# Optimization experiments

Hardware: AMD Instinct MI355X
Metric: run time of the kernel (lower is better)

The kernel has to match this reference:

```python
import jax, jax.numpy as jnp
import numpy as np

B, N, C, K = 4, 1024, 384, 10


def _sqdist(a, b):
    # a: [B,P,3], b: [B,M,3] -> [B,P,M] squared euclidean distance
    d = (jnp.sum(a * a, -1)[:, :, None] + jnp.sum(b * b, -1)[:, None, :]
         - 2.0 * jnp.einsum('bpc,bmc->bpm', a, b))
    return jnp.maximum(d, 0.0)


def _gather(points, idx):
    # points: [B,M,C], idx: [B,...] int -> [B,...,C]  (index_points)
    return jax.vmap(lambda p, i: p[i])(points, idx)


def setup_inputs() -> dict:
    key = jax.random.key(0)
    ks = jax.random.split(key, 8)
    def lin(k_, fan_in, fan_out):
        return jax.random.normal(k_, (fan_in, fan_out), jnp.float32) * (1.0 / np.sqrt(fan_in))
    return {
        'q': jax.random.normal(ks[0], (B, N, C), jnp.float32),
        'q_pos': jax.random.normal(ks[1], (B, N, 3), jnp.float32),
        'Wv': lin(ks[2], C, C), 'bv': jnp.zeros((C,), jnp.float32),
        'W1': lin(ks[3], 2 * C, C), 'b1': jnp.zeros((C,), jnp.float32),
        'ln_g': jnp.ones((C,), jnp.float32), 'ln_b': jnp.zeros((C,), jnp.float32),
        'W2': lin(ks[4], C, 3),
        'Wk': lin(ks[5], 2 * C, C), 'bk': jnp.zeros((C,), jnp.float32),
    }


def reference(q, q_pos, Wv, bv, W1, b1, ln_g, ln_b, W2, Wk, bk):
    Bq, Nq, Cq = q.shape
    # 1) KNN of each query among all points (self-attn: v=q, v_pos=q_pos)
    d = _sqdist(q_pos, q_pos)                      # [B,N,N]
    _, idx = jax.lax.top_k(-d, K)                  # [B,N,K] (smallest distances)
    # 2) offset prediction from gathered projected features + query feature
    v_off = q @ Wv + bv                            # [B,N,C]
    off_local_v = _gather(v_off, idx)              # [B,N,K,C]
    qk = jnp.broadcast_to(q[:, :, None, :], (Bq, Nq, K, Cq))
    shift_feat = jnp.concatenate([off_local_v, qk], -1)  # [B,N,K,2C]
    h = shift_feat @ W1 + b1
    mu = jnp.mean(h, -1, keepdims=True)
    var = jnp.var(h, -1, keepdims=True)
    h = (h - mu) / jnp.sqrt(var + 1e-5) * ln_g + ln_b     # LayerNorm
    h = jax.nn.gelu(h, approximate=False)
    offset = jnp.tanh(h @ W2)                      # [B,N,K,3]
    # 3) deformed positions, scaled by half the local bbox extent
    local_v_pos = _gather(q_pos, idx)              # [B,N,K,3]
    scale = (local_v_pos.max(-2) - local_v_pos.min(-2))[:, :, None, :] * 0.5
    shift_pos = (local_v_pos + offset * scale).reshape(Bq, Nq * K, 3)
    # 4) three_nn + three_interpolate (inverse-squared-distance weights)
    d2 = _sqdist(shift_pos, q_pos)                 # [B,NK,N]
    negd, idx3 = jax.lax.top_k(-d2, 3)             # [B,NK,3]
    dist = -negd
    w = 1.0 / (dist + 1e-8)
    w = w / jnp.sum(w, -1, keepdims=True)
    feats3 = _gather(q, idx3)                      # [B,NK,3,C]
    interp = jnp.einsum('bpt,bptc->bpc', w, feats3).reshape(Bq, Nq, K, Cq)
    # 5) graph conv: concat(diff, q) -> Linear -> LeakyReLU(0.2) -> max over K
    feature = jnp.concatenate([interp - qk, qk], -1)      # [B,N,K,2C]
    out = jax.nn.leaky_relu(feature @ Wk + bk, negative_slope=0.2)
    return out.max(-2)                             # [B,N,C]
```

## Files before the change

### kernel.cpp

```cpp
#include <hip/hip_runtime.h>
#include <math.h>

#define BB 4
#define NN 1024
#define CC 384
#define KK 10
#define NKK (NN*KK)

typedef __attribute__((ext_vector_type(8))) short short8v;
typedef __attribute__((ext_vector_type(8))) unsigned short ushort8v;
typedef __attribute__((ext_vector_type(4))) float f32x4;

template <int NA>
__device__ __forceinline__ void wave_sum_arr(float* a) {
  #pragma unroll
  for (int off = 32; off > 0; off >>= 1) {
    float t[NA];
    #pragma unroll
    for (int u = 0; u < NA; ++u) t[u] = __shfl_xor(a[u], off, 64);
    #pragma unroll
    for (int u = 0; u < NA; ++u) a[u] += t[u];
  }
}

__device__ __forceinline__ unsigned short f2bf(float x) {
  unsigned int b = __float_as_uint(x);
  return (unsigned short)((b + 0x7fffu + ((b >> 16) & 1u)) >> 16);
}
__device__ __forceinline__ float bf2f(unsigned short h) {
  return __uint_as_float(((unsigned int)h) << 16);
}

#define NB_CVT  (BB * NN * CC / 1024)
#define NB_PB   (2 * CC * CC / 256)
#define NB_PREP (NB_CVT + NB_PB + 3)
__global__ __launch_bounds__(256) void prep_gemm_kernel(
    const float* __restrict__ q,
    const float* __restrict__ W1, const float* __restrict__ b1,
    const float* __restrict__ bv, const float* __restrict__ bk,
    const float* __restrict__ Wk, const float* __restrict__ Wv,
    unsigned short* __restrict__ qh, unsigned short* __restrict__ ql,
    unsigned short* __restrict__ Wt,
    float* __restrict__ bias_uv, float* __restrict__ bias_pb,
    float* __restrict__ M1p) {
  int blk = blockIdx.x;
  int tid = threadIdx.x;
  if (blk < NB_CVT) {
    int i = (blk * 256 + tid) * 4;
    float4 v = *reinterpret_cast<const float4*>(q + i);
    float x[4] = {v.x, v.y, v.z, v.w};
    #pragma unroll
    for (int j = 0; j < 4; ++j) {
      unsigned short h = f2bf(x[j]);
      qh[i + j] = h;
      ql[i + j] = f2bf(x[j] - bf2f(h));
    }
    return;
  }
  if (blk < NB_CVT + NB_PB) {
    int idx = (blk - NB_CVT) * 256 + tid;
    int n = idx / CC, k = idx % CC;
    float v;
    if (n < CC) v = Wk[(size_t)k * CC + n];
    else        v = Wk[(size_t)CC * CC + k * CC + (n - CC)] - Wk[(size_t)k * CC + (n - CC)];
    Wt[(size_t)n * CC + k] = f2bf(v);
    return;
  }
  if (blk < NB_PREP) {
    int j = (blk - NB_CVT - NB_PB) * 256 + tid;
    if (j >= 2 * CC) return;
    if (j < CC) { bias_uv[j] = 0.f; bias_pb[j] = 0.f; }
    else {
      int c = j - CC;
      float s = b1[c];
      for (int i = 0; i < CC; ++i) s += bv[i] * W1[i * CC + c];
      bias_uv[j] = s;
      bias_pb[j] = bk[c];
    }
    return;
  }
  {
    int r = blk - NB_PREP;
    int bx = r % 3, by = (r / 3) % 3, bz = r / 9;
    __shared__ float As[16][132];
    __shared__ float Bs[16][128];
    int tx = tid & 15, ty = tid >> 4;
    int row0 = by * 128, col0 = bx * 128;
    int k0 = bz * 48;
    float acc[8][8] = {};
    int arow = tid >> 2, akc = (tid & 3) << 2;
    int brow = tid >> 5, bcol = (tid & 31) << 2;
    for (int kt = k0; kt < k0 + 48; kt += 16) {
      #pragma unroll
      for (int h = 0; h < 2; ++h) {
        int rr = arow + 64 * h;
        float4 av = *reinterpret_cast<const float4*>(Wv + (size_t)(row0 + rr) * CC + kt + akc);
        As[akc + 0][rr] = av.x; As[akc + 1][rr] = av.y;
        As[akc + 2][rr] = av.z; As[akc + 3][rr] = av.w;
      }
      #pragma unroll
      for (int h = 0; h < 2; ++h) {
        int rr = brow + 8 * h;
        float4 bv4 = *reinterpret_cast<const float4*>(W1 + (size_t)(kt + rr) * CC + col0 + bcol);
        *reinterpret_cast<float4*>(&Bs[rr][bcol]) = bv4;
      }
      __syncthreads();
      #pragma unroll
      for (int kk = 0; kk < 16; ++kk) {
        float4 a0 = *reinterpret_cast<const float4*>(&As[kk][ty << 2]);
        float4 a1 = *reinterpret_cast<const float4*>(&As[kk][64 + (ty << 2)]);
        float4 b0 = *reinterpret_cast<const float4*>(&Bs[kk][tx << 2]);
        float4 b1 = *reinterpret_cast<const float4*>(&Bs[kk][64 + (tx << 2)]);
        float av_[8] = {a0.x, a0.y, a0.z, a0.w, a1.x, a1.y, a1.z, a1.w};
        float bv_[8] = {b0.x, b0.y, b0.z, b0.w, b1.x, b1.y, b1.z, b1.w};
        #pragma unroll
        for (int i = 0; i < 8; ++i)
          #pragma unroll
          for (int j = 0; j < 8; ++j) acc[i][j] += av_[i] * bv_[j];
      }
      __syncthreads();
    }
    float* Cz = M1p + (size_t)bz * CC * CC;
    #pragma unroll
    for (int i = 0; i < 8; ++i) {
      int row = row0 + (ty << 2) + (i & 3) + ((i & 4) << 4);
      if (row >= CC) continue;
      #pragma unroll
      for (int h = 0; h < 2; ++h) {
        int col = col0 + 64 * h + (tx << 2);
        if (col >= CC) continue;
        float4 rv;
        rv.x = acc[i][4 * h + 0]; rv.y = acc[i][4 * h + 1];
        rv.z = acc[i][4 * h + 2]; rv.w = acc[i][4 * h + 3];
        *reinterpret_cast<float4*>(Cz + (size_t)row * CC + col) = rv;
      }
    }
  }
}

__global__ void pack_uv_split_kernel(const float* __restrict__ M1p, const float* __restrict__ W1,
                                     unsigned short* __restrict__ Buvh,
                                     unsigned short* __restrict__ Buvl) {
  int idx = blockIdx.x * 256 + threadIdx.x;
  int k = idx / (2 * CC), n = idx % (2 * CC);
  float val;
  if (n < CC) {
    float s = 0.f;
    #pragma unroll
    for (int p = 0; p < 8; ++p) s += M1p[(size_t)p * CC * CC + (size_t)k * CC + n];
    val = s;
  } else {
    val = W1[(size_t)(CC + k) * CC + (n - CC)];
  }
  unsigned short h = f2bf(val);
  Buvh[(size_t)n * CC + k] = h;
  Buvl[(size_t)n * CC + k] = f2bf(val - bf2f(h));
}

__global__ __launch_bounds__(256) void gemm_mfma_kernel(
    const unsigned short* __restrict__ qh, const unsigned short* __restrict__ ql,
    const unsigned short* __restrict__ Buvh, const unsigned short* __restrict__ Buvl,
    const unsigned short* __restrict__ Wt,
    float* __restrict__ Cuv, float* __restrict__ Cpb,
    const float* __restrict__ bias_uv, const float* __restrict__ bias_pb) {
  int path = blockIdx.z;
  const unsigned short* Bh = path ? Wt : Buvh;
  float* Cm = path ? Cpb : Cuv;
  const float* bias = path ? bias_pb : bias_uv;
  __shared__ unsigned short Ah[128 * 32], Alo[128 * 32];
  __shared__ unsigned short Bhs[128 * 32], Bls[128 * 32];
  int tid = threadIdx.x;
  int lane = tid & 63, w = tid >> 6;
  int m0 = blockIdx.y * 128, n0 = blockIdx.x * 128;
  f32x4 acc[4][4];
  #pragma unroll
  for (int i = 0; i < 4; ++i)
    #pragma unroll
    for (int j = 0; j < 4; ++j) acc[i][j] = (f32x4){0.f, 0.f, 0.f, 0.f};
  int rl = lane & 15, kg = lane >> 4;
  for (int k0 = 0; k0 < CC; k0 += 32) {
    #pragma unroll
    for (int j = 0; j < 2; ++j) {
      int id = tid + 256 * j;
      int r = id >> 2, s = id & 3;
      int sw = (s ^ (r & 3)) * 8;
      *reinterpret_cast<ushort8v*>(Ah + r * 32 + sw) =
          *reinterpret_cast<const ushort8v*>(qh + (size_t)(m0 + r) * CC + k0 + s * 8);
      *reinterpret_cast<ushort8v*>(Bhs + r * 32 + sw) =
          *reinterpret_cast<const ushort8v*>(Bh + (size_t)(n0 + r) * CC + k0 + s * 8);
      if (!path) {
        *reinterpret_cast<ushort8v*>(Alo + r * 32 + sw) =
            *reinterpret_cast<const ushort8v*>(ql + (size_t)(m0 + r) * CC + k0 + s * 8);
        *reinterpret_cast<ushort8v*>(Bls + r * 32 + sw) =
            *reinterpret_cast<const ushort8v*>(Buvl + (size_t)(n0 + r) * CC + k0 + s * 8);
      }
    }
    __syncthreads();
    short8v afh[4], bfh[4], afl[4], bfl[4];
    #pragma unroll
    for (int f = 0; f < 4; ++f) {
      int ar = (w & 1) * 64 + f * 16 + rl;
      int aof = ar * 32 + (kg ^ (ar & 3)) * 8;
      int br = (w >> 1) * 64 + f * 16 + rl;
      int bof = br * 32 + (kg ^ (br & 3)) * 8;
      afh[f] = *reinterpret_cast<const short8v*>(Ah + aof);
      bfh[f] = *reinterpret_cast<const short8v*>(Bhs + bof);
      if (!path) {
        afl[f] = *reinterpret_cast<const short8v*>(Alo + aof);
        bfl[f] = *reinterpret_cast<const short8v*>(Bls + bof);
      }
    }
    #pragma unroll
    for (int i = 0; i < 4; ++i) {
      #pragma unroll
      for (int j = 0; j < 4; ++j) {
        acc[i][j] = __builtin_amdgcn_mfma_f32_16x16x32_bf16(afh[i], bfh[j], acc[i][j], 0, 0, 0);
        if (!path) {
          acc[i][j] = __builtin_amdgcn_mfma_f32_16x16x32_bf16(afh[i], bfl[j], acc[i][j], 0, 0, 0);
          acc[i][j] = __builtin_amdgcn_mfma_f32_16x16x32_bf16(afl[i], bfh[j], acc[i][j], 0, 0, 0);
        }
      }
    }
    __syncthreads();
  }
  #pragma unroll
  for (int i = 0; i < 4; ++i) {
    #pragma unroll
    for (int j = 0; j < 4; ++j) {
      int col = n0 + (w >> 1) * 64 + j * 16 + rl;
      float bcol_v = bias[col];
      #pragma unroll
      for (int r = 0; r < 4; ++r) {
        int row = m0 + (w & 1) * 64 + i * 16 + kg * 4 + r;
        Cm[(size_t)row * (2 * CC) + col] = acc[i][j][r] + bcol_v;
      }
    }
  }
}

__global__ __launch_bounds__(256) void tail_kernel(
    const float* __restrict__ Cat_uv, const float* __restrict__ Cat_pb,
    const float* __restrict__ lng, const float* __restrict__ lnb,
    const float* __restrict__ W2, const float* __restrict__ q_pos,
    float* __restrict__ out) {
  int bn = blockIdx.x;
  int b = bn >> 10, n = bn & (NN - 1);
  int tid = threadIdx.x;
  int wave = tid >> 6, lane = tid & 63;
  __shared__ float4 sp4[NN];
  __shared__ int s_nb[KK];
  __shared__ float s_scale[3], s_lvp[KK][3];
  __shared__ float s_shp[KK][3];
  __shared__ float s_w[KK][3];
  __shared__ int s_i[KK][3];

  const float* qp = q_pos + (size_t)b * NN * 3;
  for (int i = tid; i < NN; i += 256) {
    float x = qp[i * 3 + 0], y = qp[i * 3 + 1], z = qp[i * 3 + 2];
    sp4[i] = (float4){x, y, z, x * x + y * y + z * z};
  }
  float Vv[6], lg[6], lb[6], w2a[6], w2b[6], w2c[6];
  const float* Vrow = Cat_uv + (size_t)bn * (2 * CC) + CC;
  #pragma unroll
  for (int i = 0; i < 6; ++i) {
    int c = lane + (i << 6);
    Vv[i] = Vrow[c];
    lg[i] = lng[c]; lb[i] = lnb[c];
    w2a[i] = W2[c * 3 + 0]; w2b[i] = W2[c * 3 + 1]; w2c[i] = W2[c * 3 + 2];
  }
  __syncthreads();

  if (wave == 0) {
    float4 me = sp4[n];
    float px = me.x, py = me.y, pz = me.z, sp = me.w;
    float bd[KK]; int bi[KK];
    #pragma unroll
    for (int s = 0; s < KK; ++s) { bd[s] = 1e30f; bi[s] = -1; }
    #pragma unroll 4
    for (int j = 0; j < 16; ++j) {
      int m = lane + (j << 6);
      float4 c = sp4[m];
      float dot = fmaf(px, c.x, fmaf(py, c.y, pz * c.z));
      float d = fmaf(-2.f, dot, sp + c.w);
      d = fmaxf(d, 0.f);
      if (d < bd[KK - 1]) {
        bd[KK - 1] = d; bi[KK - 1] = m;
        #pragma unroll
        for (int s = KK - 1; s >= 1; --s) {
          if (bd[s] < bd[s - 1]) {
            float td = bd[s]; bd[s] = bd[s - 1]; bd[s - 1] = td;
            int ti = bi[s]; bi[s] = bi[s - 1]; bi[s - 1] = ti;
          }
        }
      }
    }
    for (int s = 0; s < KK; ++s) {
      float d = bd[0]; int i = bi[0];
      #pragma unroll
      for (int off = 32; off > 0; off >>= 1) {
        float od = __shfl_xor(d, off, 64);
        int oi = __shfl_xor(i, off, 64);
        if (od < d || (od == d && oi < i)) { d = od; i = oi; }
      }
      if (bi[0] == i) {
        #pragma unroll
        for (int u = 0; u < KK - 1; ++u) { bd[u] = bd[u + 1]; bi[u] = bi[u + 1]; }
        bd[KK - 1] = 1e30f; bi[KK - 1] = -1;
      }
      if (lane == 0) s_nb[s] = i;
    }
  }
  __syncthreads();

  if (tid < 3) {
    float mx = -1e30f, mn = 1e30f;
    #pragma unroll
    for (int k2 = 0; k2 < KK; ++k2) {
      const float* c = (const float*)&sp4[s_nb[k2]];
      float v = c[tid];
      mx = fmaxf(mx, v); mn = fminf(mn, v);
      s_lvp[k2][tid] = v;
    }
    s_scale[tid] = (mx - mn) * 0.5f;
  }
  __syncthreads();

  {
    int nk = (wave < 2) ? 3 : 2;
    int kb = (wave < 2) ? wave * 3 : 6 + (wave - 2) * 2;
    float hk[3][6];
    float sum[3];
    #pragma unroll
    for (int kk = 0; kk < 3; ++kk) {
      int k = kb + (kk < nk ? kk : nk - 1);
      const float* Urow = Cat_uv + ((size_t)b * NN + s_nb[k]) * (2 * CC);
      float s = 0.f;
      #pragma unroll
      for (int i = 0; i < 6; ++i) {
        hk[kk][i] = Urow[lane + (i << 6)] + Vv[i];
        s += hk[kk][i];
      }
      sum[kk] = s;
    }
    wave_sum_arr<3>(sum);
    float mu[3], var[3];
    #pragma unroll
    for (int kk = 0; kk < 3; ++kk) {
      mu[kk] = sum[kk] * (1.0f / CC);
      float v = 0.f;
      #pragma unroll
      for (int i = 0; i < 6; ++i) { float d = hk[kk][i] - mu[kk]; v += d * d; }
      var[kk] = v;
    }
    wave_sum_arr<3>(var);
    float o[9];
    #pragma unroll
    for (int kk = 0; kk < 3; ++kk) {
      float rstd = 1.0f / sqrtf(var[kk] * (1.0f / CC) + 1e-5f);
      float o0 = 0.f, o1 = 0.f, o2 = 0.f;
      #pragma unroll
      for (int i = 0; i < 6; ++i) {
        float x = (hk[kk][i] - mu[kk]) * rstd * lg[i] + lb[i];
        float g = 0.5f * x * (1.0f + erff(x * 0.70710678118654752440f));
        o0 = fmaf(g, w2a[i], o0); o1 = fmaf(g, w2b[i], o1); o2 = fmaf(g, w2c[i], o2);
      }
      o[kk * 3 + 0] = o0; o[kk * 3 + 1] = o1; o[kk * 3 + 2] = o2;
    }
    wave_sum_arr<9>(o);
    if (lane == 0) {
      #pragma unroll
      for (int kk = 0; kk < 3; ++kk) {
        if (kk < nk) {
          int k = kb + kk;
          s_shp[k][0] = s_lvp[k][0] + tanhf(o[kk * 3 + 0]) * s_scale[0];
          s_shp[k][1] = s_lvp[k][1] + tanhf(o[kk * 3 + 1]) * s_scale[1];
          s_shp[k][2] = s_lvp[k][2] + tanhf(o[kk * 3 + 2]) * s_scale[2];
        }
      }
    }
  }
  __syncthreads();

  for (int pi = 0; pi < 3; ++pi) {
    int p = wave + pi * 4;
    if (p >= KK) break;
    float px = s_shp[p][0], py = s_shp[p][1], pz = s_shp[p][2];
    float sp = fmaf(px, px, fmaf(py, py, pz * pz));
    float d0 = 1e30f, d1 = 1e30f, d2 = 1e30f;
    int i0 = -1, i1 = -1, i2 = -1;
    #pragma unroll 4
    for (int j = 0; j < 16; ++j) {
      int m = lane + (j << 6);
      float4 c = sp4[m];
      float dot = fmaf(px, c.x, fmaf(py, c.y, pz * c.z));
      float d = fmaf(-2.f, dot, sp + c.w);
      d = fmaxf(d, 0.f);
      bool c2 = d < d2, c1 = d < d1, c0 = d < d0;
      d2 = c1 ? d1 : (c2 ? d : d2);  i2 = c1 ? i1 : (c2 ? m : i2);
      d1 = c0 ? d0 : (c1 ? d : d1);  i1 = c0 ? i0 : (c1 ? m : i1);
      d0 = c0 ? d : d0;              i0 = c0 ? m : i0;
    }
    float wd[3]; int wi[3];
    #pragma unroll
    for (int s = 0; s < 3; ++s) {
      float d = d0; int i = i0;
      #pragma unroll
      for (int off = 32; off > 0; off >>= 1) {
        float od = __shfl_xor(d, off, 64);
        int oi = __shfl_xor(i, off, 64);
        if (od < d || (od == d && oi < i)) { d = od; i = oi; }
      }
      if (i0 == i) { d0 = d1; i0 = i1; d1 = d2; i1 = i2; d2 = 1e30f; i2 = -1; }
      wd[s] = d; wi[s] = i;
    }
    if (lane == 0) {
      float w0 = 1.f / (wd[0] + 1e-8f), w1 = 1.f / (wd[1] + 1e-8f), w2 = 1.f / (wd[2] + 1e-8f);
      float s = w0 + w1 + w2;
      s_w[p][0] = w0 / s; s_w[p][1] = w1 / s; s_w[p][2] = w2 / s;
      s_i[p][0] = wi[0];  s_i[p][1] = wi[1];  s_i[p][2] = wi[2];
    }
  }
  __syncthreads();

  const float* Pb = Cat_pb + (size_t)b * NN * (2 * CC);
  const float* BseRow = Cat_pb + (size_t)bn * (2 * CC) + CC;
  for (int c = tid; c < CC; c += 256) {
    float base = BseRow[c];
    float best = -1e30f;
    #pragma unroll
    for (int k = 0; k < KK; ++k) {
      float acc = base;
      #pragma unroll
      for (int tt = 0; tt < 3; ++tt)
        acc = fmaf(s_w[k][tt], Pb[(size_t)s_i[k][tt] * (2 * CC) + c], acc);
      acc = acc >= 0.f ? acc : 0.2f * acc;
      best = fmaxf(best, acc);
    }
    out[(size_t)bn * CC + c] = best;
  }
}

extern "C" void kernel_launch(void* const* d_in, const int* in_sizes, int n_in,
                              void* d_out, int out_size, void* d_ws, size_t ws_size,
                              hipStream_t stream) {
  (void)in_sizes; (void)n_in; (void)out_size; (void)ws_size;
  const float* q    = (const float*)d_in[0];
  const float* qpos = (const float*)d_in[1];
  const float* Wv   = (const float*)d_in[2];
  const float* bv   = (const float*)d_in[3];
  const float* W1   = (const float*)d_in[4];
  const float* b1   = (const float*)d_in[5];
  const float* lng  = (const float*)d_in[6];
  const float* lnb  = (const float*)d_in[7];
  const float* W2   = (const float*)d_in[8];
  const float* Wk   = (const float*)d_in[9];
  const float* bk   = (const float*)d_in[10];
  float* out = (float*)d_out;

  float* ws = (float*)d_ws;
  float* Cat_uv = ws; ws += (size_t)BB * NN * 2 * CC;
  float* Cat_pb = ws; ws += (size_t)BB * NN * 2 * CC;
  float* M1p = Cat_pb;
  float* bias_uv = ws; ws += 2 * CC;
  float* bias_pb = ws; ws += 2 * CC;
  unsigned short* qh = (unsigned short*)ws;  ws += (size_t)BB * NN * CC / 2;
  unsigned short* ql = (unsigned short*)ws;  ws += (size_t)BB * NN * CC / 2;
  unsigned short* Wt = (unsigned short*)ws;  ws += (size_t)2 * CC * CC / 2;
  unsigned short* Buvh = (unsigned short*)ws; ws += (size_t)2 * CC * CC / 2;
  unsigned short* Buvl = (unsigned short*)ws; ws += (size_t)2 * CC * CC / 2;

  prep_gemm_kernel<<<dim3(NB_PREP + 72), dim3(256), 0, stream>>>(
      q, W1, b1, bv, bk, Wk, Wv, qh, ql, Wt, bias_uv, bias_pb, M1p);
  pack_uv_split_kernel<<<dim3(CC * 2 * CC / 256), dim3(256), 0, stream>>>(M1p, W1, Buvh, Buvl);
  gemm_mfma_kernel<<<dim3(2 * CC / 128, BB * NN / 128, 2), dim3(256), 0, stream>>>(
      qh, ql, Buvh, Buvl, Wt, Cat_uv, Cat_pb, bias_uv, bias_pb);
  tail_kernel<<<dim3(BB * NN), dim3(256), 0, stream>>>(
      Cat_uv, Cat_pb, lng, lnb, W2, qpos, out);
}
```

Baseline: 161.4 us.

## Process four query points per tail block, one wave per point

The tail kernel is restructured so each 256-thread block handles four query points, with each wave owning one point end to end (KNN, offset MLP, three_nn, interpolation). Before, one block handled a single point and only wave 0 did the KNN while the other waves sat idle. The change also amortises the per-block load of the 1024 positions into shared memory over four points and removes several block-wide barriers. In exchange each wave now runs all ten neighbours serially, with larger register arrays (for example 15-wide reductions), which may raise register pressure and lower occupancy.

After: 171.6 us. 6.4% more time.

```diff
diff --git a/kernel.cpp b/kernel.cpp
--- a/kernel.cpp
+++ b/kernel.cpp
@@ -243,16 +243,18 @@
     const float* __restrict__ lng, const float* __restrict__ lnb,
     const float* __restrict__ W2, const float* __restrict__ q_pos,
     float* __restrict__ out) {
-  int bn = blockIdx.x;
-  int b = bn >> 10, n = bn & (NN - 1);
+  int blk = blockIdx.x;
+  int b = blk >> 8;
+  int ng = blk & 255;
   int tid = threadIdx.x;
   int wave = tid >> 6, lane = tid & 63;
+  int n = ng * 4 + wave;
+  int bn = b * NN + n;
   __shared__ float4 sp4[NN];
-  __shared__ int s_nb[KK];
-  __shared__ float s_scale[3], s_lvp[KK][3];
-  __shared__ float s_shp[KK][3];
-  __shared__ float s_w[KK][3];
-  __shared__ int s_i[KK][3];
+  __shared__ int s_nb[4][KK];
+  __shared__ float s_shp[4][KK][3];
+  __shared__ float s_w[4][KK][3];
+  __shared__ int s_i[4][KK][3];
 
   const float* qp = q_pos + (size_t)b * NN * 3;
   for (int i = tid; i < NN; i += 256) {
@@ -270,7 +272,7 @@
   }
   __syncthreads();
 
-  if (wave == 0) {
+  {
     float4 me = sp4[n];
     float px = me.x, py = me.y, pz = me.z, sp = me.w;
     float bd[KK]; int bi[KK];
@@ -307,33 +309,35 @@
         for (int u = 0; u < KK - 1; ++u) { bd[u] = bd[u + 1]; bi[u] = bi[u + 1]; }
         bd[KK - 1] = 1e30f; bi[KK - 1] = -1;
       }
-      if (lane == 0) s_nb[s] = i;
+      if (lane == 0) s_nb[wave][s] = i;
     }
   }
   __syncthreads();
 
-  if (tid < 3) {
-    float mx = -1e30f, mn = 1e30f;
+  int nb[KK];
+  #pragma unroll
+  for (int s = 0; s < KK; ++s) nb[s] = s_nb[wave][s];
+  float sclx, scly, sclz;
+  {
+    float mxx = -1e30f, mnx = 1e30f, mxy = -1e30f, mny = 1e30f, mxz = -1e30f, mnz = 1e30f;
     #pragma unroll
     for (int k2 = 0; k2 < KK; ++k2) {
-      const float* c = (const float*)&sp4[s_nb[k2]];
-      float v = c[tid];
-      mx = fmaxf(mx, v); mn = fminf(mn, v);
-      s_lvp[k2][tid] = v;
-    }
-    s_scale[tid] = (mx - mn) * 0.5f;
-  }
-  __syncthreads();
-
-  {
-    int nk = (wave < 2) ? 3 : 2;
-    int kb = (wave < 2) ? wave * 3 : 6 + (wave - 2) * 2;
-    float hk[3][6];
-    float sum[3];
-    #pragma unroll
-    for (int kk = 0; kk < 3; ++kk) {
-      int k = kb + (kk < nk ? kk : nk - 1);
-      const float* Urow = Cat_uv + ((size_t)b * NN + s_nb[k]) * (2 * CC);
+      float4 c = sp4[nb[k2]];
+      mxx = fmaxf(mxx, c.x); mnx = fminf(mnx, c.x);
+      mxy = fmaxf(mxy, c.y); mny = fminf(mny, c.y);
+      mxz = fmaxf(mxz, c.z); mnz = fminf(mnz, c.z);
+    }
+    sclx = (mxx - mnx) * 0.5f; scly = (mxy - mny) * 0.5f; sclz = (mxz - mnz) * 0.5f;
+  }
+
+  #pragma unroll
+  for (int half = 0; half < 2; ++half) {
+    int kb = half * 5;
+    float hk[5][6];
+    float sum[5];
+    #pragma unroll
+    for (int kk = 0; kk < 5; ++kk) {
+      const float* Urow = Cat_uv + ((size_t)b * NN + nb[kb + kk]) * (2 * CC);
       float s = 0.f;
       #pragma unroll
       for (int i = 0; i < 6; ++i) {
@@ -342,20 +346,20 @@
       }
       sum[kk] = s;
     }
-    wave_sum_arr<3>(sum);
-    float mu[3], var[3];
-    #pragma unroll
-    for (int kk = 0; kk < 3; ++kk) {
+    wave_sum_arr<5>(sum);
+    float mu[5], var[5];
+    #pragma unroll
+    for (int kk = 0; kk < 5; ++kk) {
       mu[kk] = sum[kk] * (1.0f / CC);
       float v = 0.f;
       #pragma unroll
       for (int i = 0; i < 6; ++i) { float d = hk[kk][i] - mu[kk]; v += d * d; }
       var[kk] = v;
     }
-    wave_sum_arr<3>(var);
-    float o[9];
-    #pragma unroll
-    for (int kk = 0; kk < 3; ++kk) {
+    wave_sum_arr<5>(var);
+    float o[15];
+    #pragma unroll
+    for (int kk = 0; kk < 5; ++kk) {
       float rstd = 1.0f / sqrtf(var[kk] * (1.0f / CC) + 1e-5f);
       float o0 = 0.f, o1 = 0.f, o2 = 0.f;
       #pragma unroll
@@ -366,25 +370,23 @@
       }
       o[kk * 3 + 0] = o0; o[kk * 3 + 1] = o1; o[kk * 3 + 2] = o2;
     }
-    wave_sum_arr<9>(o);
+    wave_sum_arr<15>(o);
     if (lane == 0) {
       #pragma unroll
-      for (int kk = 0; kk < 3; ++kk) {
-        if (kk < nk) {
-          int k = kb + kk;
-          s_shp[k][0] = s_lvp[k][0] + tanhf(o[kk * 3 + 0]) * s_scale[0];
-          s_shp[k][1] = s_lvp[k][1] + tanhf(o[kk * 3 + 1]) * s_scale[1];
-          s_shp[k][2] = s_lvp[k][2] + tanhf(o[kk * 3 + 2]) * s_scale[2];
-        }
+      for (int kk = 0; kk < 5; ++kk) {
+        int k = kb + kk;
+        float4 lv = sp4[nb[k]];
+        s_shp[wave][k][0] = lv.x + tanhf(o[kk * 3 + 0]) * sclx;
+        s_shp[wave][k][1] = lv.y + tanhf(o[kk * 3 + 1]) * scly;
+        s_shp[wave][k][2] = lv.z + tanhf(o[kk * 3 + 2]) * sclz;
       }
     }
   }
   __syncthreads();
 
-  for (int pi = 0; pi < 3; ++pi) {
-    int p = wave + pi * 4;
-    if (p >= KK) break;
-    float px = s_shp[p][0], py = s_shp[p][1], pz = s_shp[p][2];
+  #pragma unroll
+  for (int p = 0; p < KK; ++p) {
+    float px = s_shp[wave][p][0], py = s_shp[wave][p][1], pz = s_shp[wave][p][2];
     float sp = fmaf(px, px, fmaf(py, py, pz * pz));
     float d0 = 1e30f, d1 = 1e30f, d2 = 1e30f;
     int i0 = -1, i1 = -1, i2 = -1;
@@ -416,15 +418,17 @@
     if (lane == 0) {
       float w0 = 1.f / (wd[0] + 1e-8f), w1 = 1.f / (wd[1] + 1e-8f), w2 = 1.f / (wd[2] + 1e-8f);
       float s = w0 + w1 + w2;
-      s_w[p][0] = w0 / s; s_w[p][1] = w1 / s; s_w[p][2] = w2 / s;
-      s_i[p][0] = wi[0];  s_i[p][1] = wi[1];  s_i[p][2] = wi[2];
+      s_w[wave][p][0] = w0 / s; s_w[wave][p][1] = w1 / s; s_w[wave][p][2] = w2 / s;
+      s_i[wave][p][0] = wi[0];  s_i[wave][p][1] = wi[1];  s_i[wave][p][2] = wi[2];
     }
   }
   __syncthreads();
 
   const float* Pb = Cat_pb + (size_t)b * NN * (2 * CC);
   const float* BseRow = Cat_pb + (size_t)bn * (2 * CC) + CC;
-  for (int c = tid; c < CC; c += 256) {
+  #pragma unroll 2
+  for (int ci = 0; ci < 6; ++ci) {
+    int c = lane + (ci << 6);
     float base = BseRow[c];
     float best = -1e30f;
     #pragma unroll
@@ -432,7 +436,7 @@
       float acc = base;
       #pragma unroll
       for (int tt = 0; tt < 3; ++tt)
-        acc = fmaf(s_w[k][tt], Pb[(size_t)s_i[k][tt] * (2 * CC) + c], acc);
+        acc = fmaf(s_w[wave][k][tt], Pb[(size_t)s_i[wave][k][tt] * (2 * CC) + c], acc);
       acc = acc >= 0.f ? acc : 0.2f * acc;
       best = fmaxf(best, acc);
     }
@@ -474,6 +478,6 @@
   pack_uv_split_kernel<<<dim3(CC * 2 * CC / 256), dim3(256), 0, stream>>>(M1p, W1, Buvh, Buvl);
   gemm_mfma_kernel<<<dim3(2 * CC / 128, BB * NN / 128, 2), dim3(256), 0, stream>>>(
       qh, ql, Buvh, Buvl, Wt, Cat_uv, Cat_pb, bias_uv, bias_pb);
-  tail_kernel<<<dim3(BB * NN), dim3(256), 0, stream>>>(
+  tail_kernel<<<dim3(BB * NN / 4), dim3(256), 0, stream>>>(
       Cat_uv, Cat_pb, lng, lnb, W2, qpos, out);
 }
```
